# Kernel tuning notes

Hardware: AMD Instinct MI355X
Metric: run time of the kernel (lower is better)

The kernel has to match this reference:

```python
import jax, jax.numpy as jnp
import numpy as np

D_MODEL = 1024
H = 16
D_K = D_MODEL // H
D_FF = 4096
EPS = 1e-6


def setup_inputs() -> dict:
    key = jax.random.key(0)
    ks = jax.random.split(key, 12)
    s = 0.02
    inp = {
        "x": jax.random.normal(ks[0], (2, 2048, D_MODEL), jnp.float32),
        # attention projection weights stored [in, out] (y = x @ W + b)
        "Wq": jax.random.normal(ks[1], (D_MODEL, D_MODEL), jnp.float32) * s,
        "bq": jnp.zeros((D_MODEL,), jnp.float32),
        "Wk": jax.random.normal(ks[2], (D_MODEL, D_MODEL), jnp.float32) * s,
        "bk": jnp.zeros((D_MODEL,), jnp.float32),
        "Wv": jax.random.normal(ks[3], (D_MODEL, D_MODEL), jnp.float32) * s,
        "bv": jnp.zeros((D_MODEL,), jnp.float32),
        "Wo": jax.random.normal(ks[4], (D_MODEL, D_MODEL), jnp.float32) * s,
        "bo": jnp.zeros((D_MODEL,), jnp.float32),
        # FFN
        "W1": jax.random.normal(ks[5], (D_MODEL, D_FF), jnp.float32) * s,
        "b1": jnp.zeros((D_FF,), jnp.float32),
        "W2": jax.random.normal(ks[6], (D_FF, D_MODEL), jnp.float32) * s,
        "b2": jnp.zeros((D_MODEL,), jnp.float32),
        # scalar LayerNorm params (as in the source: nn.Parameter(torch.ones(1)))
        "ln1_alpha": jnp.ones((1,), jnp.float32),
        "ln1_beta": jnp.ones((1,), jnp.float32),
        "ln2_alpha": jnp.ones((1,), jnp.float32),
        "ln2_beta": jnp.ones((1,), jnp.float32),
    }
    return inp


def _layernorm(x, alpha, beta):
    # Faithful to source: unbiased std (ddof=1), divide by (std + eps)
    mean = jnp.mean(x, axis=-1, keepdims=True)
    var = jnp.var(x, axis=-1, keepdims=True, ddof=1)
    std = jnp.sqrt(var)
    return alpha * (x - mean) / (std + EPS) + beta


def _mha(x, Wq, bq, Wk, bk, Wv, bv, Wo, bo):
    B, S, _ = x.shape
    q = (x @ Wq + bq).reshape(B, S, H, D_K).transpose(0, 2, 1, 3)
    k = (x @ Wk + bk).reshape(B, S, H, D_K).transpose(0, 2, 1, 3)
    v = (x @ Wv + bv).reshape(B, S, H, D_K).transpose(0, 2, 1, 3)
    # NOTE: source has no 1/sqrt(d_k) scaling
    scores = jnp.einsum('bhqd,bhkd->bhqk', q, k)
    attn = jax.nn.softmax(scores, axis=-1)
    out = jnp.einsum('bhqk,bhkd->bhqd', attn, v)
    out = out.transpose(0, 2, 1, 3).reshape(B, S, D_MODEL)
    return out @ Wo + bo


def reference(x, Wq, bq, Wk, bk, Wv, bv, Wo, bo, W1, b1, W2, b2,
              ln1_alpha, ln1_beta, ln2_alpha, ln2_beta):
    # pre-norm residual 1: self-attention (dropout=0, eval mode)
    h = x + _mha(_layernorm(x, ln1_alpha, ln1_beta), Wq, bq, Wk, bk, Wv, bv, Wo, bo)
    # pre-norm residual 2: FFN
    n = _layernorm(h, ln2_alpha, ln2_beta)
    ffn = jax.nn.relu(n @ W1 + b1) @ W2 + b2
    return h + ffn
```

## Files before the change

kernel.cpp:

```cpp
#include <hip/hip_runtime.h>

#define DMODEL 1024
#define DFF    4096
#define SEQ    2048
#define NTOK   4096
#define QKVN   3072
#define LOG2E  1.4426950408889634f

typedef unsigned short u16;
typedef short s8v __attribute__((ext_vector_type(8)));
typedef float f4v __attribute__((ext_vector_type(4)));

__device__ __forceinline__ u16 f2bf(float f) {
  union { float f; unsigned u; } c; c.f = f;
  unsigned r = c.u + 0x7fffu + ((c.u >> 16) & 1u);
  return (u16)(r >> 16);
}
__device__ __forceinline__ float u2f(unsigned u) {
  union { unsigned u; float f; } c; c.u = u; return c.f;
}

__device__ __forceinline__ unsigned cvt_pk_bf16(float lo, float hi) {
  unsigned r;
  asm("v_cvt_pk_bf16_f32 %0, %1, %2" : "=v"(r) : "v"(lo), "v"(hi));
  return r;
}
__device__ __forceinline__ void pl32swap(unsigned& x, unsigned& y) {
  asm("v_permlane32_swap_b32 %0, %1" : "+v"(x), "+v"(y));
}
__device__ __forceinline__ void pl16swap(unsigned& x, unsigned& y) {
  asm("v_permlane16_swap_b32 %0, %1" : "+v"(x), "+v"(y));
}

typedef const __attribute__((address_space(1))) unsigned GAS;
typedef __attribute__((address_space(3))) unsigned LAS;
__device__ __forceinline__ void gl2lds16(const void* g, void* l) {
  __builtin_amdgcn_global_load_lds((GAS*)g, (LAS*)l, 16, 0, 0);
}

__device__ __forceinline__ void tr32(const float* __restrict__ W, u16* __restrict__ Wt,
                                     int K, int N, int bx, int by, float (*sh)[33],
                                     float scale) {
  int n0 = bx * 32, k0 = by * 32;
  int tx = threadIdx.x & 31, ty = threadIdx.x >> 5;
#pragma unroll
  for (int r = ty; r < 32; r += 8) sh[r][tx] = W[(size_t)(k0 + r) * N + n0 + tx];
  __syncthreads();
#pragma unroll
  for (int r = ty; r < 32; r += 8) Wt[(size_t)(n0 + r) * K + k0 + tx] = f2bf(sh[tx][r] * scale);
}

__global__ __launch_bounds__(256)
void prep(const float* __restrict__ Wq, const float* __restrict__ Wk,
          const float* __restrict__ Wv, const float* __restrict__ Wo,
          const float* __restrict__ W1, const float* __restrict__ W2,
          const float* __restrict__ bq, const float* __restrict__ bk,
          const float* __restrict__ bv,
          u16* __restrict__ wqkv_t, u16* __restrict__ wo_t,
          u16* __restrict__ w1_t, u16* __restrict__ w2_t, float* __restrict__ bqkv) {
  __shared__ float sh[32][33];
  int b = blockIdx.x;
  if (b < 1024) {
    tr32(Wq, wqkv_t, 1024, 1024, b & 31, b >> 5, sh, LOG2E);
  } else if (b < 2048) {
    b -= 1024; tr32(Wk, wqkv_t + (1u << 20), 1024, 1024, b & 31, b >> 5, sh, 1.0f);
  } else if (b < 3072) {
    b -= 2048; tr32(Wv, wqkv_t + (2u << 20), 1024, 1024, b & 31, b >> 5, sh, 1.0f);
  } else if (b < 4096) {
    b -= 3072; tr32(Wo, wo_t, 1024, 1024, b & 31, b >> 5, sh, 1.0f);
  } else if (b < 8192) {
    b -= 4096; tr32(W1, w1_t, 1024, 4096, b & 127, b >> 7, sh, 1.0f);
  } else if (b < 12288) {
    b -= 8192; tr32(W2, w2_t, 4096, 1024, b & 31, b >> 5, sh, 1.0f);
  } else {
    int t = (b - 12288) * 256 + threadIdx.x;
    float v = (t < 1024) ? bq[t] * LOG2E : (t < 2048 ? bk[t - 1024] : bv[t - 2048]);
    bqkv[t] = v;
  }
}

__global__ __launch_bounds__(256)
void ln_bf16(const float* __restrict__ X, u16* __restrict__ Y,
             const float* __restrict__ a_p, const float* __restrict__ b_p) {
  int row = blockIdx.x;
  const float4* xr = (const float4*)(X + (size_t)row * DMODEL);
  float4 v = xr[threadIdx.x];
  float s  = v.x + v.y + v.z + v.w;
  float ss = v.x * v.x + v.y * v.y + v.z * v.z + v.w * v.w;
#pragma unroll
  for (int m = 32; m >= 1; m >>= 1) { s += __shfl_xor(s, m, 64); ss += __shfl_xor(ss, m, 64); }
  __shared__ float red[8];
  int wid = threadIdx.x >> 6, lane = threadIdx.x & 63;
  if (lane == 0) { red[wid] = s; red[4 + wid] = ss; }
  __syncthreads();
  s  = red[0] + red[1] + red[2] + red[3];
  ss = red[4] + red[5] + red[6] + red[7];
  float mean = s * (1.0f / 1024.0f);
  float var  = fmaxf((ss - s * mean) * (1.0f / 1023.0f), 0.0f);
  float k    = a_p[0] / (sqrtf(var) + 1e-6f);
  float beta = b_p[0];
  ushort4 o;
  o.x = f2bf((v.x - mean) * k + beta);
  o.y = f2bf((v.y - mean) * k + beta);
  o.z = f2bf((v.z - mean) * k + beta);
  o.w = f2bf((v.w - mean) * k + beta);
  ((ushort4*)(Y + (size_t)row * DMODEL))[threadIdx.x] = o;
}

template <int RELU, int RESID, int OUT_BF16, int ATOMIC>
__global__ __launch_bounds__(256, 3)
void gemm_bt(const u16* __restrict__ A, const u16* __restrict__ Bt,
             const float* __restrict__ bias, const float* __restrict__ resid,
             void* __restrict__ Cout, int M, int N, int K) {
  __shared__ __align__(16) u16 As[128 * 64];
  __shared__ __align__(16) u16 Bs[128 * 64];
  const int lane = threadIdx.x & 63, wid = threadIdx.x >> 6;
  const int llo = lane & 15, lhi = lane >> 4;
  const int m0 = blockIdx.y * 128, n0 = blockIdx.x * 128;
  const int wm = wid & 1, wn = wid >> 1;
  const int r8 = lane >> 3;
  const int c8 = ((lane & 7) ^ r8) * 8;

  f4v acc[4][4];
  const f4v fz = {0.f, 0.f, 0.f, 0.f};
#pragma unroll
  for (int i = 0; i < 4; ++i)
#pragma unroll
    for (int j = 0; j < 4; ++j) acc[i][j] = fz;

  const u16* Ag = A  + (size_t)(m0 + r8) * K + c8;
  const u16* Bg = Bt + (size_t)(n0 + r8) * K + c8;

  const int Kp = ATOMIC ? (K / gridDim.z) : K;
  const int kbeg = ATOMIC ? blockIdx.z * Kp : 0;
  const int kend = kbeg + Kp;

  for (int kt = kbeg; kt < kend; kt += 64) {
#pragma unroll
    for (int c = 0; c < 4; ++c) {
      int ch = wid * 4 + c;
      gl2lds16(Ag + (size_t)(ch * 8) * K + kt, As + ch * 512);
      gl2lds16(Bg + (size_t)(ch * 8) * K + kt, Bs + ch * 512);
    }
    __syncthreads();
#pragma unroll
    for (int ks = 0; ks < 2; ++ks) {
      const int so = ((ks * 4 + lhi) ^ (llo & 7)) * 8;
      s8v a[4], b[4];
#pragma unroll
      for (int i = 0; i < 4; ++i)
        a[i] = *(const s8v*)&As[(wm * 64 + i * 16 + llo) * 64 + so];
#pragma unroll
      for (int j = 0; j < 4; ++j)
        b[j] = *(const s8v*)&Bs[(wn * 64 + j * 16 + llo) * 64 + so];
#pragma unroll
      for (int i = 0; i < 4; ++i)
#pragma unroll
        for (int j = 0; j < 4; ++j)
          acc[i][j] = __builtin_amdgcn_mfma_f32_16x16x32_bf16(a[i], b[j], acc[i][j], 0, 0, 0);
    }
    __syncthreads();
  }
#pragma unroll
  for (int j = 0; j < 4; ++j) {
    int col = n0 + wn * 64 + j * 16 + llo;
    float bv = bias[col];
#pragma unroll
    for (int i = 0; i < 4; ++i) {
      int r0 = m0 + wm * 64 + i * 16 + lhi * 4;
#pragma unroll
      for (int r = 0; r < 4; ++r) {
        size_t idx = (size_t)(r0 + r) * N + col;
        float v = acc[i][j][r];
        if (ATOMIC) {
          if (blockIdx.z == 0) {
            v += bv;
            if (RESID) v += resid[idx];
          }
          atomicAdd(&((float*)Cout)[idx], v);
        } else {
          v += bv;
          if (RESID) v += resid[idx];
          if (RELU) v = fmaxf(v, 0.0f);
          if (OUT_BF16) ((u16*)Cout)[idx] = f2bf(v);
          else          ((float*)Cout)[idx] = v;
        }
      }
    }
  }
}

__global__ __launch_bounds__(256, 3)
void flash_attn(const u16* __restrict__ QKV, u16* __restrict__ Pacc,
                float* __restrict__ Pml) {
  __shared__ __align__(16) u16 smem[16896];
  u16* Ks = smem;
  u16* Vt = smem + 8192;

  const int tid = threadIdx.x;
  const int lane = tid & 63, wid = tid >> 6;
  const int llo = lane & 15, lhi = lane >> 4;
  const int qt = blockIdx.x, bh = blockIdx.y, z = blockIdx.z;
  const int b = bh >> 4, h = bh & 15;
  const int LDM = QKVN;
  const size_t base = (size_t)b * SEQ * LDM + h * 64;
  const u16* Qb = QKV + base + (size_t)qt * 128 * LDM;
  const u16* Kb = QKV + base + 1024;
  const u16* Vb = QKV + base + 2048;
  const int r8 = lane >> 3;
  const int c8 = ((lane & 7) ^ r8) * 8;

#pragma unroll
  for (int c = 0; c < 4; ++c) {
    int ch = wid * 4 + c;
    gl2lds16(Qb + (size_t)(ch * 8 + r8) * LDM + c8, Ks + ch * 512);
  }
  __syncthreads();
  s8v qf[2][2];
#pragma unroll
  for (int mb = 0; mb < 2; ++mb)
#pragma unroll
    for (int ks = 0; ks < 2; ++ks)
      qf[mb][ks] = *(const s8v*)&Ks[(wid * 32 + mb * 16 + llo) * 64 +
                                    (((ks * 4 + lhi) ^ (llo & 7)) * 8)];
  __syncthreads();

  f4v accO[2][4];
  float l_run[2] = {0.f, 0.f};
  const f4v fz = {0.f, 0.f, 0.f, 0.f};
#pragma unroll
  for (int mb = 0; mb < 2; ++mb)
#pragma unroll
    for (int db = 0; db < 4; ++db) accO[mb][db] = fz;

  for (int kt = z * 8; kt < z * 8 + 8; ++kt) {
#pragma unroll
    for (int c = 0; c < 4; ++c) {
      int ch = wid * 4 + c;
      gl2lds16(Kb + (size_t)(kt * 128 + ch * 8 + r8) * LDM + c8, Ks + ch * 512);
    }
#pragma unroll
    for (int it = 0; it < 2; ++it) {
      int o  = wid + it * 4;
      int k2 = lane * 2;
      const u16* vp = Vb + (size_t)(kt * 128 + k2) * LDM + o * 8;
      s8v v0 = *(const s8v*)vp;
      s8v v1 = *(const s8v*)(vp + LDM);
      const u16* e0 = (const u16*)&v0;
      const u16* e1 = (const u16*)&v1;
#pragma unroll
      for (int j = 0; j < 8; ++j) {
        unsigned pk = (unsigned)e0[j] | ((unsigned)e1[j] << 16);
        *(unsigned*)&Vt[(o * 8 + j) * 136 + k2] = pk;
      }
    }
    __syncthreads();

    s8v pa[2][4];
#pragma unroll
    for (int ksb = 0; ksb < 4; ++ksb) {
      f4v sA[2], sB[2];
#pragma unroll
      for (int mb = 0; mb < 2; ++mb) { sA[mb] = fz; sB[mb] = fz; }
#pragma unroll
      for (int ks = 0; ks < 2; ++ks) {
        const int so = ((ks * 4 + lhi) ^ (llo & 7)) * 8;
        s8v kfA = *(const s8v*)&Ks[((ksb * 2 + 0) * 16 + llo) * 64 + so];
        s8v kfB = *(const s8v*)&Ks[((ksb * 2 + 1) * 16 + llo) * 64 + so];
#pragma unroll
        for (int mb = 0; mb < 2; ++mb) {
          sA[mb] = __builtin_amdgcn_mfma_f32_16x16x32_bf16(kfA, qf[mb][ks], sA[mb], 0, 0, 0);
          sB[mb] = __builtin_amdgcn_mfma_f32_16x16x32_bf16(kfB, qf[mb][ks], sB[mb], 0, 0, 0);
        }
      }
#pragma unroll
      for (int mb = 0; mb < 2; ++mb) {
        float pA0 = __builtin_amdgcn_exp2f(sA[mb][0]);
        float pA1 = __builtin_amdgcn_exp2f(sA[mb][1]);
        float pA2 = __builtin_amdgcn_exp2f(sA[mb][2]);
        float pA3 = __builtin_amdgcn_exp2f(sA[mb][3]);
        float pB0 = __builtin_amdgcn_exp2f(sB[mb][0]);
        float pB1 = __builtin_amdgcn_exp2f(sB[mb][1]);
        float pB2 = __builtin_amdgcn_exp2f(sB[mb][2]);
        float pB3 = __builtin_amdgcn_exp2f(sB[mb][3]);
        l_run[mb] += ((pA0 + pA1) + (pA2 + pA3)) + ((pB0 + pB1) + (pB2 + pB3));
        unsigned a0 = cvt_pk_bf16(pA0, pA1), a1 = cvt_pk_bf16(pA2, pA3);
        unsigned b0 = cvt_pk_bf16(pB0, pB1), b1 = cvt_pk_bf16(pB2, pB3);
        pl32swap(a0, b0); pl16swap(a0, b0);
        pl32swap(a1, b1); pl16swap(a1, b1);
        union { unsigned u[4]; s8v v; } pk;
        pk.u[0] = a0; pk.u[1] = a1; pk.u[2] = b0; pk.u[3] = b1;
        pa[mb][ksb] = pk.v;
      }
    }

#pragma unroll
    for (int ks = 0; ks < 4; ++ks) {
      s8v vb2[4];
#pragma unroll
      for (int db = 0; db < 4; ++db)
        vb2[db] = *(const s8v*)&Vt[(db * 16 + llo) * 136 + ks * 32 + lhi * 8];
#pragma unroll
      for (int mb = 0; mb < 2; ++mb)
#pragma unroll
        for (int db = 0; db < 4; ++db)
          accO[mb][db] = __builtin_amdgcn_mfma_f32_16x16x32_bf16(pa[mb][ks], vb2[db], accO[mb][db], 0, 0, 0);
    }
    __syncthreads();
  }

#pragma unroll
  for (int mb = 0; mb < 2; ++mb) {
    l_run[mb] += __shfl_xor(l_run[mb], 16, 64);
    l_run[mb] += __shfl_xor(l_run[mb], 32, 64);
  }
#pragma unroll
  for (int mb = 0; mb < 2; ++mb) {
    int row0 = qt * 128 + wid * 32 + mb * 16;
    size_t ibase = (size_t)(z * 32 + bh) * SEQ + row0;
    if (lane < 16) Pml[ibase + lane] = l_run[mb];
#pragma unroll
    for (int r = 0; r < 4; ++r) {
      size_t irow = ibase + lhi * 4 + r;
#pragma unroll
      for (int db = 0; db < 4; ++db)
        Pacc[irow * 64 + db * 16 + llo] = f2bf(accO[mb][db][r]);
    }
  }
}

__global__ __launch_bounds__(256)
void attn_combine(const u16* __restrict__ Pacc, const float* __restrict__ Pml,
                  u16* __restrict__ ctx) {
  int g = blockIdx.x * 256 + threadIdx.x;
  int d2 = g & 31;
  int row = (g >> 5) & (SEQ - 1);
  int bh = g >> 16;
  int b = bh >> 4, h = bh & 15;
  size_t i0 = (size_t)bh * SEQ + row;
  size_t i1 = (size_t)(32 + bh) * SEQ + row;
  float inv = 1.0f / (Pml[i0] + Pml[i1]);
  unsigned pa = ((const unsigned*)Pacc)[i0 * 32 + d2];
  unsigned pb = ((const unsigned*)Pacc)[i1 * 32 + d2];
  float lo = u2f(pa << 16) + u2f(pb << 16);
  float hi = u2f(pa & 0xffff0000u) + u2f(pb & 0xffff0000u);
  unsigned o = (unsigned)f2bf(lo * inv) | ((unsigned)f2bf(hi * inv) << 16);
  ((unsigned*)ctx)[(size_t)(b * SEQ + row) * (DMODEL / 2) + h * 32 + d2] = o;
}

extern "C" void kernel_launch(void* const* d_in, const int* in_sizes, int n_in,
                              void* d_out, int out_size, void* d_ws, size_t ws_size,
                              hipStream_t stream) {
  const float* x   = (const float*)d_in[0];
  const float* Wq  = (const float*)d_in[1];  const float* bq = (const float*)d_in[2];
  const float* Wk  = (const float*)d_in[3];  const float* bk = (const float*)d_in[4];
  const float* Wv  = (const float*)d_in[5];  const float* bv = (const float*)d_in[6];
  const float* Wo  = (const float*)d_in[7];  const float* bo = (const float*)d_in[8];
  const float* W1  = (const float*)d_in[9];  const float* b1 = (const float*)d_in[10];
  const float* W2  = (const float*)d_in[11]; const float* b2 = (const float*)d_in[12];
  const float* l1a = (const float*)d_in[13]; const float* l1b = (const float*)d_in[14];
  const float* l2a = (const float*)d_in[15]; const float* l2b = (const float*)d_in[16];

  char* ws = (char*)d_ws;
  const size_t MB = 1u << 20;
  u16*   wqkv_t = (u16*)(ws + 0);
  u16*   wo_t   = (u16*)(ws + 6 * MB);
  u16*   w1_t   = (u16*)(ws + 8 * MB);
  u16*   w2_t   = (u16*)(ws + 16 * MB);
  float* bqkv   = (float*)(ws + 24 * MB);
  u16*   xn1    = (u16*)(ws + 25 * MB);
  u16*   qkv    = (u16*)(ws + 33 * MB);
  u16*   ctx    = (u16*)(ws + 57 * MB);
  float* hbuf   = (float*)(ws + 65 * MB);
  u16*   Pacc   = (u16*)(ws + 81 * MB);
  float* Pml    = (float*)(ws + 97 * MB);
  u16*   n2     = (u16*)(ws + 81 * MB);
  u16*   mid    = (u16*)(ws + 25 * MB);

  dim3 blk(256);

  hipMemsetAsync(d_out, 0, (size_t)NTOK * DMODEL * 4, stream);
  hipMemsetAsync(hbuf, 0, (size_t)NTOK * DMODEL * 4, stream);

  prep<<<dim3(12300), blk, 0, stream>>>(Wq, Wk, Wv, Wo, W1, W2, bq, bk, bv,
                                        wqkv_t, wo_t, w1_t, w2_t, bqkv);

  ln_bf16<<<NTOK, blk, 0, stream>>>(x, xn1, l1a, l1b);

  gemm_bt<0, 0, 1, 0><<<dim3(24, 32), blk, 0, stream>>>(xn1, wqkv_t, bqkv, nullptr, qkv,
                                                        NTOK, QKVN, DMODEL);

  flash_attn<<<dim3(16, 32, 2), blk, 0, stream>>>(qkv, Pacc, Pml);
  attn_combine<<<dim3(8192), blk, 0, stream>>>(Pacc, Pml, ctx);

  gemm_bt<0, 1, 0, 1><<<dim3(8, 32, 2), blk, 0, stream>>>(ctx, wo_t, bo, x, hbuf,
                                                          NTOK, DMODEL, DMODEL);

  ln_bf16<<<NTOK, blk, 0, stream>>>(hbuf, n2, l2a, l2b);

  gemm_bt<1, 0, 1, 0><<<dim3(32, 32), blk, 0, stream>>>(n2, w1_t, b1, nullptr, mid,
                                                        NTOK, DFF, DMODEL);

  gemm_bt<0, 1, 0, 1><<<dim3(8, 32, 2), blk, 0, stream>>>(mid, w2_t, b2, hbuf, (float*)d_out,
                                                          NTOK, DMODEL, DFF);
}
```

Measured before the change: 396.2 us.

## Double-buffer GEMM LDS tiles and remap workgroups for XCD-aware L2 locality

The GEMM kernel now keeps two LDS buffers, so the global-to-LDS load of the next K tile is issued before the MFMA work on the current tile, with one barrier per iteration. Launch bounds drop from 3 to 2 blocks per SM to make room for the doubled shared memory. Both the GEMM and flash-attention kernels remap their linear block index so that consecutive tiles land on the same XCD (stride-8 interleave), aiming for better L2 reuse of shared operands. The cost is lower occupancy and a remap that assumes 8 XCDs and, in attention, a fixed 16x32 grid shape.

```diff
diff --git a/kernel.cpp b/kernel.cpp
--- a/kernel.cpp
+++ b/kernel.cpp
@@ -108,15 +108,20 @@
 }
 
 template <int RELU, int RESID, int OUT_BF16, int ATOMIC>
-__global__ __launch_bounds__(256, 3)
+__global__ __launch_bounds__(256, 2)
 void gemm_bt(const u16* __restrict__ A, const u16* __restrict__ Bt,
              const float* __restrict__ bias, const float* __restrict__ resid,
              void* __restrict__ Cout, int M, int N, int K) {
-  __shared__ __align__(16) u16 As[128 * 64];
-  __shared__ __align__(16) u16 Bs[128 * 64];
+  __shared__ __align__(16) u16 As[2][128 * 64];
+  __shared__ __align__(16) u16 Bs[2][128 * 64];
   const int lane = threadIdx.x & 63, wid = threadIdx.x >> 6;
   const int llo = lane & 15, lhi = lane >> 4;
-  const int m0 = blockIdx.y * 128, n0 = blockIdx.x * 128;
+
+  const int nwg = gridDim.x * gridDim.y;
+  int lin = blockIdx.y * gridDim.x + blockIdx.x;
+  if ((nwg & 7) == 0) lin = (lin & 7) * (nwg >> 3) + (lin >> 3);
+  const int m0 = (lin / gridDim.x) * 128, n0 = (lin % gridDim.x) * 128;
+
   const int wm = wid & 1, wn = wid >> 1;
   const int r8 = lane >> 3;
   const int c8 = ((lane & 7) ^ r8) * 8;
@@ -133,33 +138,40 @@
 
   const int Kp = ATOMIC ? (K / gridDim.z) : K;
   const int kbeg = ATOMIC ? blockIdx.z * Kp : 0;
-  const int kend = kbeg + Kp;
-
-  for (int kt = kbeg; kt < kend; kt += 64) {
+  const int nk = Kp >> 6;
+
+  auto stage = [&](int buf, int kt) {
 #pragma unroll
     for (int c = 0; c < 4; ++c) {
       int ch = wid * 4 + c;
-      gl2lds16(Ag + (size_t)(ch * 8) * K + kt, As + ch * 512);
-      gl2lds16(Bg + (size_t)(ch * 8) * K + kt, Bs + ch * 512);
-    }
-    __syncthreads();
+      gl2lds16(Ag + (size_t)(ch * 8) * K + kt, As[buf] + ch * 512);
+      gl2lds16(Bg + (size_t)(ch * 8) * K + kt, Bs[buf] + ch * 512);
+    }
+  };
+
+  stage(0, kbeg);
+  __syncthreads();
+  int cur = 0;
+  for (int i = 0; i < nk; ++i) {
+    if (i + 1 < nk) stage(cur ^ 1, kbeg + (i + 1) * 64);
 #pragma unroll
     for (int ks = 0; ks < 2; ++ks) {
       const int so = ((ks * 4 + lhi) ^ (llo & 7)) * 8;
       s8v a[4], b[4];
 #pragma unroll
-      for (int i = 0; i < 4; ++i)
-        a[i] = *(const s8v*)&As[(wm * 64 + i * 16 + llo) * 64 + so];
+      for (int ii = 0; ii < 4; ++ii)
+        a[ii] = *(const s8v*)&As[cur][(wm * 64 + ii * 16 + llo) * 64 + so];
 #pragma unroll
       for (int j = 0; j < 4; ++j)
-        b[j] = *(const s8v*)&Bs[(wn * 64 + j * 16 + llo) * 64 + so];
-#pragma unroll
-      for (int i = 0; i < 4; ++i)
+        b[j] = *(const s8v*)&Bs[cur][(wn * 64 + j * 16 + llo) * 64 + so];
+#pragma unroll
+      for (int ii = 0; ii < 4; ++ii)
 #pragma unroll
         for (int j = 0; j < 4; ++j)
-          acc[i][j] = __builtin_amdgcn_mfma_f32_16x16x32_bf16(a[i], b[j], acc[i][j], 0, 0, 0);
+          acc[ii][j] = __builtin_amdgcn_mfma_f32_16x16x32_bf16(a[ii], b[j], acc[ii][j], 0, 0, 0);
     }
     __syncthreads();
+    cur ^= 1;
   }
 #pragma unroll
   for (int j = 0; j < 4; ++j) {
@@ -200,7 +212,9 @@
   const int tid = threadIdx.x;
   const int lane = tid & 63, wid = tid >> 6;
   const int llo = lane & 15, lhi = lane >> 4;
-  const int qt = blockIdx.x, bh = blockIdx.y, z = blockIdx.z;
+  int lin = blockIdx.y * 16 + blockIdx.x;
+  lin = (lin & 7) * 64 + (lin >> 3);
+  const int qt = lin & 15, bh = lin >> 4, z = blockIdx.z;
   const int b = bh >> 4, h = bh & 15;
   const int LDM = QKVN;
   const size_t base = (size_t)b * SEQ * LDM + h * 64;
```

Measured after the change: 398.4 us. Within noise of the previous version (+0.5%).

## Add 256x256 double-buffered GEMM for QKV/FFN1 and XCD-aware block remapping

Applied to the files above, without the earlier changes.

Adds a 512-thread gemm256 kernel with 256x256 output tiles and double-buffered LDS staging, and uses it for the QKV projection and the first FFN matmul. This raises operand reuse per tile and overlaps global loads with MFMA work. It also remaps workgroup IDs across the 8 XCDs in both GEMMs and in flash attention, so that neighbouring tiles share an L2. The trade-off is fewer blocks: 192 and 256 workgroups on 256 CUs, which leaves CUs underused and makes tail effects more likely, plus 128 KB of LDS per block.

```diff
diff --git a/kernel.cpp b/kernel.cpp
--- a/kernel.cpp
+++ b/kernel.cpp
@@ -116,7 +116,12 @@
   __shared__ __align__(16) u16 Bs[128 * 64];
   const int lane = threadIdx.x & 63, wid = threadIdx.x >> 6;
   const int llo = lane & 15, lhi = lane >> 4;
-  const int m0 = blockIdx.y * 128, n0 = blockIdx.x * 128;
+
+  const int nwg = gridDim.x * gridDim.y;
+  int lin = blockIdx.y * gridDim.x + blockIdx.x;
+  if ((nwg & 7) == 0) lin = (lin & 7) * (nwg >> 3) + (lin >> 3);
+  const int m0 = (lin / gridDim.x) * 128, n0 = (lin % gridDim.x) * 128;
+
   const int wm = wid & 1, wn = wid >> 1;
   const int r8 = lane >> 3;
   const int c8 = ((lane & 7) ^ r8) * 8;
@@ -190,6 +195,87 @@
   }
 }
 
+template <int RELU, int OUT_BF16>
+__global__ __launch_bounds__(512, 2)
+void gemm256(const u16* __restrict__ A, const u16* __restrict__ Bt,
+             const float* __restrict__ bias, void* __restrict__ Cout,
+             int M, int N, int K) {
+  __shared__ __align__(16) u16 As[2][256 * 64];
+  __shared__ __align__(16) u16 Bs[2][256 * 64];
+  const int lane = threadIdx.x & 63, wid = threadIdx.x >> 6;
+  const int llo = lane & 15, lhi = lane >> 4;
+  const int wr = wid >> 2, wc = wid & 3;
+
+  const int nwg = gridDim.x * gridDim.y;
+  int lin = blockIdx.y * gridDim.x + blockIdx.x;
+  if ((nwg & 7) == 0) lin = (lin & 7) * (nwg >> 3) + (lin >> 3);
+  const int m0 = (lin / gridDim.x) * 256, n0 = (lin % gridDim.x) * 256;
+
+  const int r8 = lane >> 3;
+  const int c8 = ((lane & 7) ^ r8) * 8;
+
+  f4v acc[8][4];
+  const f4v fz = {0.f, 0.f, 0.f, 0.f};
+#pragma unroll
+  for (int i = 0; i < 8; ++i)
+#pragma unroll
+    for (int j = 0; j < 4; ++j) acc[i][j] = fz;
+
+  const u16* Ag = A  + (size_t)(m0 + r8) * K + c8;
+  const u16* Bg = Bt + (size_t)(n0 + r8) * K + c8;
+  const int nk = K >> 6;
+
+  auto stage = [&](int buf, int kt) {
+#pragma unroll
+    for (int c = 0; c < 4; ++c) {
+      int ch = wid * 4 + c;
+      gl2lds16(Ag + (size_t)(ch * 8) * K + kt, As[buf] + ch * 512);
+      gl2lds16(Bg + (size_t)(ch * 8) * K + kt, Bs[buf] + ch * 512);
+    }
+  };
+
+  stage(0, 0);
+  __syncthreads();
+  int cur = 0;
+  for (int t = 0; t < nk; ++t) {
+    if (t + 1 < nk) stage(cur ^ 1, (t + 1) * 64);
+#pragma unroll
+    for (int ks = 0; ks < 2; ++ks) {
+      const int so = ((ks * 4 + lhi) ^ (llo & 7)) * 8;
+      s8v b[4];
+#pragma unroll
+      for (int j = 0; j < 4; ++j)
+        b[j] = *(const s8v*)&Bs[cur][(wc * 64 + j * 16 + llo) * 64 + so];
+#pragma unroll
+      for (int i = 0; i < 8; ++i) {
+        s8v a = *(const s8v*)&As[cur][(wr * 128 + i * 16 + llo) * 64 + so];
+#pragma unroll
+        for (int j = 0; j < 4; ++j)
+          acc[i][j] = __builtin_amdgcn_mfma_f32_16x16x32_bf16(a, b[j], acc[i][j], 0, 0, 0);
+      }
+    }
+    __syncthreads();
+    cur ^= 1;
+  }
+#pragma unroll
+  for (int j = 0; j < 4; ++j) {
+    int col = n0 + wc * 64 + j * 16 + llo;
+    float bv = bias[col];
+#pragma unroll
+    for (int i = 0; i < 8; ++i) {
+      int r0 = m0 + wr * 128 + i * 16 + lhi * 4;
+#pragma unroll
+      for (int r = 0; r < 4; ++r) {
+        size_t idx = (size_t)(r0 + r) * N + col;
+        float v = acc[i][j][r] + bv;
+        if (RELU) v = fmaxf(v, 0.0f);
+        if (OUT_BF16) ((u16*)Cout)[idx] = f2bf(v);
+        else          ((float*)Cout)[idx] = v;
+      }
+    }
+  }
+}
+
 __global__ __launch_bounds__(256, 3)
 void flash_attn(const u16* __restrict__ QKV, u16* __restrict__ Pacc,
                 float* __restrict__ Pml) {
@@ -200,7 +286,9 @@
   const int tid = threadIdx.x;
   const int lane = tid & 63, wid = tid >> 6;
   const int llo = lane & 15, lhi = lane >> 4;
-  const int qt = blockIdx.x, bh = blockIdx.y, z = blockIdx.z;
+  int lin = blockIdx.y * 16 + blockIdx.x;
+  lin = (lin & 7) * 64 + (lin >> 3);
+  const int qt = lin & 15, bh = lin >> 4, z = blockIdx.z;
   const int b = bh >> 4, h = bh & 15;
   const int LDM = QKVN;
   const size_t base = (size_t)b * SEQ * LDM + h * 64;
@@ -387,7 +475,7 @@
 
   ln_bf16<<<NTOK, blk, 0, stream>>>(x, xn1, l1a, l1b);
 
-  gemm_bt<0, 0, 1, 0><<<dim3(24, 32), blk, 0, stream>>>(xn1, wqkv_t, bqkv, nullptr, qkv,
+  gemm256<0, 1><<<dim3(12, 16), dim3(512), 0, stream>>>(xn1, wqkv_t, bqkv, qkv,
                                                         NTOK, QKVN, DMODEL);
 
   flash_attn<<<dim3(16, 32, 2), blk, 0, stream>>>(qkv, Pacc, Pml);
@@ -398,7 +486,7 @@
 
   ln_bf16<<<NTOK, blk, 0, stream>>>(hbuf, n2, l2a, l2b);
 
-  gemm_bt<1, 0, 1, 0><<<dim3(32, 32), blk, 0, stream>>>(n2, w1_t, b1, nullptr, mid,
+  gemm256<1, 1><<<dim3(16, 16), dim3(512), 0, stream>>>(n2, w1_t, b1, mid,
                                                         NTOK, DFF, DMODEL);
 
   gemm_bt<0, 1, 0, 1><<<dim3(8, 32, 2), blk, 0, stream>>>(mid, w2_t, b2, hbuf, (float*)d_out,
```

After: 394.4 us. Within noise of the previous version (-0.5%).
